# Kernel tuning notes

Hardware: AMD Instinct MI355X
Metric: run time of the kernel (lower is better)

The kernel has to match this reference:

```python
import jax, jax.numpy as jnp
import numpy as np

N, E, D, ED, L, B = 100000, 1600000, 128, 16, 5, 64
EPS = 1e-5


def _layer_norm(x, w, b):
    mu = jnp.mean(x, axis=-1, keepdims=True)
    var = jnp.mean((x - mu) ** 2, axis=-1, keepdims=True)
    return (x - mu) * jax.lax.rsqrt(var + EPS) * w + b


def setup_inputs() -> dict:
    key = jax.random.key(0)
    ks = jax.random.split(key, 10)
    sc = 0.05
    s = jax.random.normal(ks[0], (N, D), jnp.float32)
    edge_index = jax.random.randint(ks[1], (2, E), 0, N, dtype=jnp.int64)
    edge_attr = jax.random.normal(ks[2], (E, ED), jnp.float32)
    batch = jnp.sort(jax.random.randint(ks[3], (N,), 0, B, dtype=jnp.int64))
    return dict(
        s=s, edge_index=edge_index, edge_attr=edge_attr, batch=batch,
        ln_w=jnp.ones((L, D), jnp.float32),
        ln_b=jnp.zeros((L, D), jnp.float32),
        eW1=jax.random.normal(ks[4], (L, 2 * D + ED, ED), jnp.float32) * sc,
        eb1=jnp.zeros((L, ED), jnp.float32),
        eW2=jax.random.normal(ks[5], (L, ED, ED), jnp.float32) * sc,
        eb2=jnp.zeros((L, ED), jnp.float32),
        nW1=jax.random.normal(ks[6], (L, D + ED, D), jnp.float32) * sc,
        nb1=jnp.zeros((L, D), jnp.float32),
        nW2=jax.random.normal(ks[7], (L, D, D), jnp.float32) * sc,
        nb2=jnp.zeros((L, D), jnp.float32),
    )


def reference(s, edge_index, edge_attr, batch, ln_w, ln_b, eW1, eb1, eW2, eb2, nW1, nb1, nW2, nb2):
    src, dst = edge_index[0], edge_index[1]
    n = s.shape[0]
    num_layers = ln_w.shape[0]
    # scatter-mean denominator (in-degree, clamped to 1)
    deg = jax.ops.segment_sum(jnp.ones((edge_index.shape[1],), s.dtype), dst, num_segments=n)
    deg = jnp.maximum(deg, 1.0)[:, None]
    for i in range(num_layers):
        # per-node LayerNorm over feature dim (vector channel is None)
        s = _layer_norm(s, ln_w[i], ln_b[i])
        # edge message: gather endpoints, concat with edge_attr -> [E, 2D+ED]
        m = jnp.concatenate([s[src], s[dst], edge_attr], axis=-1)
        edge_attr = jax.nn.silu(m @ eW1[i] + eb1[i]) @ eW2[i] + eb2[i]
        # scatter-mean aggregate to destination nodes -> [N, ED]
        agg = jax.ops.segment_sum(edge_attr, dst, num_segments=n) / deg
        h = jnp.concatenate([s, agg], axis=-1)
        out = jax.nn.silu(h @ nW1[i] + nb1[i]) @ nW2[i] + nb2[i]  # discarded, as in original
    return s, edge_attr
```

## Files before the change

kernel.cpp:

```cpp
#include <hip/hip_runtime.h>

#define N_NODES 100000
#define N_EDGES 1600000
#define DIM     128
#define EDIM    16
#define NLAYERS 5

typedef unsigned short ushort_t;
typedef short bf16x8 __attribute__((ext_vector_type(8)));
typedef float f32x4  __attribute__((ext_vector_type(4)));

__device__ __forceinline__ ushort_t f2bf(float f) {
    union { float f; unsigned int i; } c; c.f = f;
    unsigned int r = c.i + 0x7fffu + ((c.i >> 16) & 1u);
    return (ushort_t)(r >> 16);
}
__device__ __forceinline__ float lo_bf(unsigned int w) {
    union { unsigned int i; float f; } c; c.i = w << 16; return c.f;
}
__device__ __forceinline__ float hi_bf(unsigned int w) {
    union { unsigned int i; float f; } c; c.i = w & 0xffff0000u; return c.f;
}
__device__ __forceinline__ unsigned int pk_bf16(float lo, float hi) {
    unsigned int r;
    asm("v_cvt_pk_bf16_f32 %0, %1, %2" : "=v"(r) : "v"(lo), "v"(hi));
    return r;
}
__device__ __forceinline__ bf16x8 pk8(f32x4 a, f32x4 b) {
    union { unsigned int w[4]; bf16x8 v; } c;
    c.w[0] = pk_bf16(a[0], a[1]); c.w[1] = pk_bf16(a[2], a[3]);
    c.w[2] = pk_bf16(b[0], b[1]); c.w[3] = pk_bf16(b[2], b[3]);
    return c.v;
}
__device__ __forceinline__ float fast_silu(float x) {
    return x * __builtin_amdgcn_rcpf(1.0f + __expf(-x));
}
__device__ __forceinline__ void lds_fence() {
    asm volatile("s_waitcnt lgkmcnt(0)" ::: "memory");
    __builtin_amdgcn_sched_barrier(0);
}

__global__ void swizzle_weights(const float* __restrict__ eW1,
                                const float* __restrict__ eW2,
                                ushort_t* __restrict__ w1s,
                                ushort_t* __restrict__ w2s) {
    int id = blockIdx.x * 256 + threadIdx.x;
    if (id >= NLAYERS * 10 * 64) return;
    int lane = id & 63;
    int t10 = id >> 6;
    int layer = t10 / 10, t = t10 % 10;
    int n = lane & 15, quad = lane >> 4;
    if (t < 9) {
        ushort_t* dst = w1s + ((size_t)(layer * 9 + t) * 64 + lane) * 8;
        #pragma unroll
        for (int j = 0; j < 8; ++j) {
            int k = t * 32 + quad * 8 + j;
            dst[j] = (k < 2 * DIM + EDIM)
                       ? f2bf(eW1[((size_t)layer * 272 + k) * 16 + n])
                       : (ushort_t)0;
        }
    } else {
        ushort_t* dst = w2s + ((size_t)layer * 64 + lane) * 8;
        #pragma unroll
        for (int j = 0; j < 8; ++j) {
            int k = quad * 8 + j;
            dst[j] = (k < EDIM) ? f2bf(eW2[((size_t)layer * 16 + k) * 16 + n])
                                : (ushort_t)0;
        }
    }
}

__global__ __launch_bounds__(256) void ln_uv(
        const float* __restrict__ sin, float* __restrict__ sout,
        const float* __restrict__ lnw, const float* __restrict__ lnb,
        const ushort_t* __restrict__ w1s,
        ushort_t* __restrict__ u_buf, ushort_t* __restrict__ v_buf,
        int l0, int l1, int lstr) {
    const int wv = threadIdx.x >> 6, lane = threadIdx.x & 63;
    const int m = lane & 15, quad = lane >> 4;
    const int tile = blockIdx.x * 4 + wv;
    if (tile >= N_NODES / 16) return;
    const int node = tile * 16 + m;

    float x[32];
    {
        const float* row = sin + (size_t)node * DIM + quad * 8;
        #pragma unroll
        for (int t = 0; t < 4; ++t) {
            f32x4 a = *(const f32x4*)(row + t * 32);
            f32x4 b = *(const f32x4*)(row + t * 32 + 4);
            #pragma unroll
            for (int j = 0; j < 4; ++j) { x[t * 8 + j] = a[j]; x[t * 8 + 4 + j] = b[j]; }
        }
    }

    for (int li = l0; li < l1; ++li) {
        float s = 0.f;
        #pragma unroll
        for (int k = 0; k < 32; ++k) s += x[k];
        s += __shfl_xor(s, 16); s += __shfl_xor(s, 32);
        float mu = s * (1.0f / DIM);
        float ss = 0.f;
        #pragma unroll
        for (int k = 0; k < 32; ++k) { float d = x[k] - mu; ss += d * d; }
        ss += __shfl_xor(ss, 16); ss += __shfl_xor(ss, 32);
        float rs = rsqrtf(ss * (1.0f / DIM) + 1e-5f);

        const float* w = lnw + (size_t)li * DIM + quad * 8;
        const float* b = lnb + (size_t)li * DIM + quad * 8;
        f32x4 au = {0.f, 0.f, 0.f, 0.f}, av = {0.f, 0.f, 0.f, 0.f};
        #pragma unroll
        for (int t = 0; t < 4; ++t) {
            f32x4 wa = *(const f32x4*)(w + t * 32), wb = *(const f32x4*)(w + t * 32 + 4);
            f32x4 ba = *(const f32x4*)(b + t * 32), bb = *(const f32x4*)(b + t * 32 + 4);
            #pragma unroll
            for (int j = 0; j < 4; ++j) {
                x[t * 8 + j]     = (x[t * 8 + j]     - mu) * rs * wa[j] + ba[j];
                x[t * 8 + 4 + j] = (x[t * 8 + 4 + j] - mu) * rs * wb[j] + bb[j];
            }
            f32x4 ya, yb;
            #pragma unroll
            for (int j = 0; j < 4; ++j) { ya[j] = x[t * 8 + j]; yb[j] = x[t * 8 + 4 + j]; }
            bf16x8 af = pk8(ya, yb);
            bf16x8 bu = *(const bf16x8*)(w1s + ((size_t)(li * 9 + t)     * 64 + lane) * 8);
            bf16x8 bv = *(const bf16x8*)(w1s + ((size_t)(li * 9 + 4 + t) * 64 + lane) * 8);
            au = __builtin_amdgcn_mfma_f32_16x16x32_bf16(bu, af, au, 0, 0, 0);
            av = __builtin_amdgcn_mfma_f32_16x16x32_bf16(bv, af, av, 0, 0, 0);
        }
        size_t rec = ((size_t)node * lstr + (li - l0)) * EDIM + quad * 4;
        uint2 tu; tu.x = pk_bf16(au[0], au[1]); tu.y = pk_bf16(au[2], au[3]);
        uint2 tv; tv.x = pk_bf16(av[0], av[1]); tv.y = pk_bf16(av[2], av[3]);
        *(uint2*)(u_buf + rec) = tu;
        *(uint2*)(v_buf + rec) = tv;
    }

    float* orow = sout + (size_t)node * DIM + quad * 8;
    #pragma unroll
    for (int t = 0; t < 4; ++t) {
        f32x4 a, b;
        #pragma unroll
        for (int j = 0; j < 4; ++j) { a[j] = x[t * 8 + j]; b[j] = x[t * 8 + 4 + j]; }
        *(f32x4*)(orow + t * 32) = a;
        *(f32x4*)(orow + t * 32 + 4) = b;
    }
}

template<int NL>
__global__ __launch_bounds__(256) void edge_fused(
        const float* __restrict__ ea_in, float* __restrict__ ea_out,
        const int* __restrict__ ei,
        const ushort_t* __restrict__ u_buf, const ushort_t* __restrict__ v_buf,
        const ushort_t* __restrict__ w1s, const ushort_t* __restrict__ w2s,
        const float* __restrict__ eb1, const float* __restrict__ eb2,
        int l0) {
    __shared__ ushort_t tbH[4][16 * 24];
    __shared__ ushort_t tbY[4][16 * 24];
    const int wv = threadIdx.x >> 6, lane = threadIdx.x & 63;
    const int m = lane & 15, quad = lane >> 4;

    bf16x8 w1f[NL], w2f[NL];
    f32x4 b1[NL], b2[NL];
    #pragma unroll
    for (int l = 0; l < NL; ++l) {
        w1f[l] = *(const bf16x8*)(w1s + (((size_t)(l0 + l) * 9 + 8) * 64 + lane) * 8);
        w2f[l] = *(const bf16x8*)(w2s + ((size_t)(l0 + l) * 64 + lane) * 8);
        #pragma unroll
        for (int r = 0; r < 4; ++r) {
            b1[l][r] = eb1[(l0 + l) * EDIM + quad * 4 + r];
            b2[l][r] = eb2[(l0 + l) * EDIM + quad * 4 + r];
        }
    }
    ushort_t* tlH = tbH[wv];
    ushort_t* tlY = tbY[wv];
    const bf16x8 zf = {0, 0, 0, 0, 0, 0, 0, 0};
    const f32x4 z4 = {0.f, 0.f, 0.f, 0.f};
    const int nTiles = N_EDGES / 64;
    const int stride = gridDim.x;

    int tile = blockIdx.x;
    if (tile >= nTiles) return;

    uint2 gu[NL], gv[NL];
    f32x4 ea_a = z4, ea_b = z4;
    int es_n, ed_n;
    {
        const int e0 = tile * 64 + wv * 16 + m;
        const int es = ei[e0];
        const int ed = ei[N_EDGES + e0];
        #pragma unroll
        for (int l = 0; l < NL; ++l) {
            gu[l] = *(const uint2*)(u_buf + ((size_t)es * NL + l) * EDIM + quad * 4);
            gv[l] = *(const uint2*)(v_buf + ((size_t)ed * NL + l) * EDIM + quad * 4);
        }
        if (quad < 2) {
            const float* ep = ea_in + (size_t)e0 * EDIM + quad * 8;
            ea_a = *(const f32x4*)ep; ea_b = *(const f32x4*)(ep + 4);
        }
        const int t1 = tile + stride;
        const int e1 = (t1 < nTiles ? t1 : tile) * 64 + wv * 16 + m;
        es_n = ei[e1];
        ed_n = ei[N_EDGES + e1];
    }

    for (; tile < nTiles; tile += stride) {
        const int tn = tile + stride;
        const bool hn = tn < nTiles;
        const int tc = hn ? tn : tile;

        uint2 gun[NL], gvn[NL];
        #pragma unroll
        for (int l = 0; l < NL; ++l) {
            gun[l] = *(const uint2*)(u_buf + ((size_t)es_n * NL + l) * EDIM + quad * 4);
            gvn[l] = *(const uint2*)(v_buf + ((size_t)ed_n * NL + l) * EDIM + quad * 4);
        }
        f32x4 ean_a = z4, ean_b = z4;
        {
            const int en = tc * 64 + wv * 16 + m;
            if (quad < 2) {
                const float* ep = ea_in + (size_t)en * EDIM + quad * 8;
                ean_a = *(const f32x4*)ep; ean_b = *(const f32x4*)(ep + 4);
            }
        }
        int es_nn, ed_nn;
        {
            const int t2 = tn + stride;
            const int e2 = (t2 < nTiles ? t2 : tc) * 64 + wv * 16 + m;
            es_nn = ei[e2];
            ed_nn = ei[N_EDGES + e2];
        }

        bf16x8 af = zf;
        if (quad < 2) af = pk8(ea_a, ea_b);

        f32x4 y = z4;
        #pragma unroll
        for (int l = 0; l < NL; ++l) {
            f32x4 acc = z4;
            acc = __builtin_amdgcn_mfma_f32_16x16x32_bf16(w1f[l], af, acc, 0, 0, 0);
            float x0 = acc[0] + lo_bf(gu[l].x) + lo_bf(gv[l].x) + b1[l][0];
            float x1 = acc[1] + hi_bf(gu[l].x) + hi_bf(gv[l].x) + b1[l][1];
            float x2 = acc[2] + lo_bf(gu[l].y) + lo_bf(gv[l].y) + b1[l][2];
            float x3 = acc[3] + hi_bf(gu[l].y) + hi_bf(gv[l].y) + b1[l][3];
            float h0 = fast_silu(x0);
            float h1 = fast_silu(x1);
            float h2 = fast_silu(x2);
            float h3 = fast_silu(x3);

            uint2 hw; hw.x = pk_bf16(h0, h1); hw.y = pk_bf16(h2, h3);
            *(uint2*)(tlH + m * 24 + quad * 4) = hw;
            lds_fence();
            bf16x8 hf = zf;
            if (quad < 2) hf = *(const bf16x8*)(tlH + m * 24 + quad * 8);

            f32x4 acc2 = z4;
            acc2 = __builtin_amdgcn_mfma_f32_16x16x32_bf16(w2f[l], hf, acc2, 0, 0, 0);
            y[0] = acc2[0] + b2[l][0];
            y[1] = acc2[1] + b2[l][1];
            y[2] = acc2[2] + b2[l][2];
            y[3] = acc2[3] + b2[l][3];

            if (l < NL - 1) {
                uint2 yw; yw.x = pk_bf16(y[0], y[1]); yw.y = pk_bf16(y[2], y[3]);
                *(uint2*)(tlY + m * 24 + quad * 4) = yw;
                lds_fence();
                af = zf;
                if (quad < 2) af = *(const bf16x8*)(tlY + m * 24 + quad * 8);
            }
        }
        const int e = tile * 64 + wv * 16 + m;
        *(f32x4*)(ea_out + (size_t)e * EDIM + quad * 4) = y;

        #pragma unroll
        for (int l = 0; l < NL; ++l) { gu[l] = gun[l]; gv[l] = gvn[l]; }
        ea_a = ean_a; ea_b = ean_b;
        es_n = es_nn; ed_n = ed_nn;
    }
}

extern "C" void kernel_launch(void* const* d_in, const int* in_sizes, int n_in,
                              void* d_out, int out_size, void* d_ws, size_t ws_size,
                              hipStream_t stream) {
    const float* s_in  = (const float*)d_in[0];
    const int*   ei    = (const int*)d_in[1];
    const float* ea_in = (const float*)d_in[2];
    const float* lnw = (const float*)d_in[4];
    const float* lnb = (const float*)d_in[5];
    const float* eW1 = (const float*)d_in[6];
    const float* eb1 = (const float*)d_in[7];
    const float* eW2 = (const float*)d_in[8];
    const float* eb2 = (const float*)d_in[9];

    float* out_s  = (float*)d_out;
    float* out_ea = (float*)d_out + (size_t)N_NODES * DIM;

    ushort_t* w1s = (ushort_t*)d_ws;
    ushort_t* w2s = w1s + (size_t)NLAYERS * 9 * 64 * 8;
    ushort_t* uv0 = w2s + (size_t)NLAYERS * 64 * 8;
    const size_t wWords  = (size_t)NLAYERS * 10 * 64 * 8;
    const size_t uvLayer = (size_t)N_NODES * EDIM;
    const size_t needFused = (wWords + 2 * (size_t)NLAYERS * uvLayer) * 2;
    const int lnGrid = (N_NODES / 16 + 3) / 4;
    const int eGrid = 4096;

    swizzle_weights<<<13, 256, 0, stream>>>(eW1, eW2, w1s, w2s);

    if (ws_size >= needFused) {
        ushort_t* u0 = uv0;
        ushort_t* v0 = u0 + (size_t)NLAYERS * uvLayer;
        ln_uv<<<lnGrid, 256, 0, stream>>>(s_in, out_s, lnw, lnb, w1s,
                                          u0, v0, 0, NLAYERS, NLAYERS);
        edge_fused<NLAYERS><<<eGrid, 256, 0, stream>>>(ea_in, out_ea, ei, u0, v0,
                                                       w1s, w2s, eb1, eb2, 0);
    } else {
        ushort_t* u0 = uv0;
        ushort_t* v0 = u0 + uvLayer;
        for (int l = 0; l < NLAYERS; ++l) {
            ln_uv<<<lnGrid, 256, 0, stream>>>(l == 0 ? s_in : out_s, out_s,
                                              lnw, lnb, w1s, u0, v0, l, l + 1, 1);
            edge_fused<1><<<eGrid, 256, 0, stream>>>(
                l == 0 ? ea_in : (const float*)out_ea, out_ea, ei, u0, v0,
                w1s, w2s, eb1, eb2, l);
        }
    }
}
```

Baseline: 434.9 us.

## Fold consecutive layer linear maps eW2·eW1_attr into combined weights

Precomputes the product of layer l's second edge linear (eW2) with layer l+1's edge-attr slice of eW1, plus the matching folded bias. The fused edge kernel then does one MFMA per layer transition instead of two, and drops one LDS round-trip and fence per layer. The folding is done once in the weight-swizzle kernel. The combined weight is rounded to bf16 after the fp32 product, which slightly changes numerics.

```diff
diff --git a/kernel.cpp b/kernel.cpp
--- a/kernel.cpp
+++ b/kernel.cpp
@@ -42,31 +42,59 @@
 
 __global__ void swizzle_weights(const float* __restrict__ eW1,
                                 const float* __restrict__ eW2,
+                                const float* __restrict__ eb1,
+                                const float* __restrict__ eb2,
                                 ushort_t* __restrict__ w1s,
-                                ushort_t* __restrict__ w2s) {
+                                ushort_t* __restrict__ w2s,
+                                ushort_t* __restrict__ wcs,
+                                float* __restrict__ bcs) {
     int id = blockIdx.x * 256 + threadIdx.x;
-    if (id >= NLAYERS * 10 * 64) return;
-    int lane = id & 63;
-    int t10 = id >> 6;
-    int layer = t10 / 10, t = t10 % 10;
-    int n = lane & 15, quad = lane >> 4;
-    if (t < 9) {
-        ushort_t* dst = w1s + ((size_t)(layer * 9 + t) * 64 + lane) * 8;
+    const int base = NLAYERS * 10 * 64;
+    if (id < base) {
+        int lane = id & 63;
+        int t10 = id >> 6;
+        int layer = t10 / 10, t = t10 % 10;
+        int n = lane & 15, quad = lane >> 4;
+        if (t < 9) {
+            ushort_t* dst = w1s + ((size_t)(layer * 9 + t) * 64 + lane) * 8;
+            #pragma unroll
+            for (int j = 0; j < 8; ++j) {
+                int k = t * 32 + quad * 8 + j;
+                dst[j] = (k < 2 * DIM + EDIM)
+                           ? f2bf(eW1[((size_t)layer * 272 + k) * 16 + n])
+                           : (ushort_t)0;
+            }
+        } else {
+            ushort_t* dst = w2s + ((size_t)layer * 64 + lane) * 8;
+            #pragma unroll
+            for (int j = 0; j < 8; ++j) {
+                int k = quad * 8 + j;
+                dst[j] = (k < EDIM) ? f2bf(eW2[((size_t)layer * 16 + k) * 16 + n])
+                                    : (ushort_t)0;
+            }
+        }
+    } else if (id < base + 4 * 64) {
+        int id2 = id - base;
+        int l = id2 >> 6;
+        int lane = id2 & 63, n = lane & 15, quad = lane >> 4;
+        ushort_t* dst = wcs + ((size_t)l * 64 + lane) * 8;
         #pragma unroll
         for (int j = 0; j < 8; ++j) {
-            int k = t * 32 + quad * 8 + j;
-            dst[j] = (k < 2 * DIM + EDIM)
-                       ? f2bf(eW1[((size_t)layer * 272 + k) * 16 + n])
-                       : (ushort_t)0;
-        }
-    } else {
-        ushort_t* dst = w2s + ((size_t)layer * 64 + lane) * 8;
-        #pragma unroll
-        for (int j = 0; j < 8; ++j) {
-            int k = quad * 8 + j;
-            dst[j] = (k < EDIM) ? f2bf(eW2[((size_t)layer * 16 + k) * 16 + n])
-                                : (ushort_t)0;
-        }
+            int r = quad * 8 + j;
+            float acc = 0.f;
+            if (r < EDIM)
+                for (int k = 0; k < EDIM; ++k)
+                    acc += eW2[((size_t)l * 16 + r) * 16 + k]
+                         * eW1[((size_t)(l + 1) * 272 + 256 + k) * 16 + n];
+            dst[j] = (r < EDIM) ? f2bf(acc) : (ushort_t)0;
+        }
+    } else if (id < base + 4 * 64 + 64) {
+        int id2 = id - base - 4 * 64;
+        int l = id2 >> 4, n = id2 & 15;
+        float acc = eb1[(l + 1) * 16 + n];
+        for (int k = 0; k < EDIM; ++k)
+            acc += eb2[l * 16 + k] * eW1[((size_t)(l + 1) * 272 + 256 + k) * 16 + n];
+        bcs[l * 16 + n] = acc;
     }
 }
 
@@ -151,27 +179,32 @@
         const int* __restrict__ ei,
         const ushort_t* __restrict__ u_buf, const ushort_t* __restrict__ v_buf,
         const ushort_t* __restrict__ w1s, const ushort_t* __restrict__ w2s,
+        const ushort_t* __restrict__ wcs, const float* __restrict__ bcs,
         const float* __restrict__ eb1, const float* __restrict__ eb2,
         int l0) {
     __shared__ ushort_t tbH[4][16 * 24];
-    __shared__ ushort_t tbY[4][16 * 24];
     const int wv = threadIdx.x >> 6, lane = threadIdx.x & 63;
     const int m = lane & 15, quad = lane >> 4;
 
-    bf16x8 w1f[NL], w2f[NL];
-    f32x4 b1[NL], b2[NL];
+    const bf16x8 w1f0 = *(const bf16x8*)(w1s + (((size_t)l0 * 9 + 8) * 64 + lane) * 8);
+    const bf16x8 w2f  = *(const bf16x8*)(w2s + ((size_t)(l0 + NL - 1) * 64 + lane) * 8);
+    bf16x8 wcf[NL > 1 ? NL - 1 : 1];
     #pragma unroll
-    for (int l = 0; l < NL; ++l) {
-        w1f[l] = *(const bf16x8*)(w1s + (((size_t)(l0 + l) * 9 + 8) * 64 + lane) * 8);
-        w2f[l] = *(const bf16x8*)(w2s + ((size_t)(l0 + l) * 64 + lane) * 8);
-        #pragma unroll
-        for (int r = 0; r < 4; ++r) {
-            b1[l][r] = eb1[(l0 + l) * EDIM + quad * 4 + r];
-            b2[l][r] = eb2[(l0 + l) * EDIM + quad * 4 + r];
-        }
-    }
+    for (int l = 1; l < NL; ++l)
+        wcf[l - 1] = *(const bf16x8*)(wcs + ((size_t)(l0 + l - 1) * 64 + lane) * 8);
+    f32x4 bx[NL], b2v;
+    #pragma unroll
+    for (int r = 0; r < 4; ++r) {
+        bx[0][r] = eb1[l0 * EDIM + quad * 4 + r];
+        b2v[r]   = eb2[(l0 + NL - 1) * EDIM + quad * 4 + r];
+    }
+    #pragma unroll
+    for (int l = 1; l < NL; ++l)
+        #pragma unroll
+        for (int r = 0; r < 4; ++r)
+            bx[l][r] = bcs[(l0 + l - 1) * EDIM + quad * 4 + r];
+
     ushort_t* tlH = tbH[wv];
-    ushort_t* tlY = tbY[wv];
     const bf16x8 zf = {0, 0, 0, 0, 0, 0, 0, 0};
     const f32x4 z4 = {0.f, 0.f, 0.f, 0.f};
     const int nTiles = N_EDGES / 64;
@@ -229,43 +262,42 @@
             ed_nn = ei[N_EDGES + e2];
         }
 
-        bf16x8 af = zf;
-        if (quad < 2) af = pk8(ea_a, ea_b);
-
-        f32x4 y = z4;
-        #pragma unroll
-        for (int l = 0; l < NL; ++l) {
-            f32x4 acc = z4;
-            acc = __builtin_amdgcn_mfma_f32_16x16x32_bf16(w1f[l], af, acc, 0, 0, 0);
-            float x0 = acc[0] + lo_bf(gu[l].x) + lo_bf(gv[l].x) + b1[l][0];
-            float x1 = acc[1] + hi_bf(gu[l].x) + hi_bf(gv[l].x) + b1[l][1];
-            float x2 = acc[2] + lo_bf(gu[l].y) + lo_bf(gv[l].y) + b1[l][2];
-            float x3 = acc[3] + hi_bf(gu[l].y) + hi_bf(gv[l].y) + b1[l][3];
-            float h0 = fast_silu(x0);
-            float h1 = fast_silu(x1);
-            float h2 = fast_silu(x2);
-            float h3 = fast_silu(x3);
-
-            uint2 hw; hw.x = pk_bf16(h0, h1); hw.y = pk_bf16(h2, h3);
+        f32x4 hv;
+        {
+            bf16x8 af = zf;
+            if (quad < 2) af = pk8(ea_a, ea_b);
+            f32x4 acc = __builtin_amdgcn_mfma_f32_16x16x32_bf16(w1f0, af, z4, 0, 0, 0);
+            hv[0] = fast_silu(acc[0] + lo_bf(gu[0].x) + lo_bf(gv[0].x) + bx[0][0]);
+            hv[1] = fast_silu(acc[1] + hi_bf(gu[0].x) + hi_bf(gv[0].x) + bx[0][1]);
+            hv[2] = fast_silu(acc[2] + lo_bf(gu[0].y) + lo_bf(gv[0].y) + bx[0][2]);
+            hv[3] = fast_silu(acc[3] + hi_bf(gu[0].y) + hi_bf(gv[0].y) + bx[0][3]);
+        }
+        #pragma unroll
+        for (int l = 1; l < NL; ++l) {
+            uint2 hw; hw.x = pk_bf16(hv[0], hv[1]); hw.y = pk_bf16(hv[2], hv[3]);
             *(uint2*)(tlH + m * 24 + quad * 4) = hw;
             lds_fence();
             bf16x8 hf = zf;
             if (quad < 2) hf = *(const bf16x8*)(tlH + m * 24 + quad * 8);
 
-            f32x4 acc2 = z4;
-            acc2 = __builtin_amdgcn_mfma_f32_16x16x32_bf16(w2f[l], hf, acc2, 0, 0, 0);
-            y[0] = acc2[0] + b2[l][0];
-            y[1] = acc2[1] + b2[l][1];
-            y[2] = acc2[2] + b2[l][2];
-            y[3] = acc2[3] + b2[l][3];
-
-            if (l < NL - 1) {
-                uint2 yw; yw.x = pk_bf16(y[0], y[1]); yw.y = pk_bf16(y[2], y[3]);
-                *(uint2*)(tlY + m * 24 + quad * 4) = yw;
-                lds_fence();
-                af = zf;
-                if (quad < 2) af = *(const bf16x8*)(tlY + m * 24 + quad * 8);
-            }
+            f32x4 acc = __builtin_amdgcn_mfma_f32_16x16x32_bf16(wcf[l - 1], hf, z4, 0, 0, 0);
+            hv[0] = fast_silu(acc[0] + lo_bf(gu[l].x) + lo_bf(gv[l].x) + bx[l][0]);
+            hv[1] = fast_silu(acc[1] + hi_bf(gu[l].x) + hi_bf(gv[l].x) + bx[l][1]);
+            hv[2] = fast_silu(acc[2] + lo_bf(gu[l].y) + lo_bf(gv[l].y) + bx[l][2]);
+            hv[3] = fast_silu(acc[3] + hi_bf(gu[l].y) + hi_bf(gv[l].y) + bx[l][3]);
+        }
+        f32x4 y;
+        {
+            uint2 hw; hw.x = pk_bf16(hv[0], hv[1]); hw.y = pk_bf16(hv[2], hv[3]);
+            *(uint2*)(tlH + m * 24 + quad * 4) = hw;
+            lds_fence();
+            bf16x8 hf = zf;
+            if (quad < 2) hf = *(const bf16x8*)(tlH + m * 24 + quad * 8);
+            f32x4 acc2 = __builtin_amdgcn_mfma_f32_16x16x32_bf16(w2f, hf, z4, 0, 0, 0);
+            y[0] = acc2[0] + b2v[0];
+            y[1] = acc2[1] + b2v[1];
+            y[2] = acc2[2] + b2v[2];
+            y[3] = acc2[3] + b2v[3];
         }
         const int e = tile * 64 + wv * 16 + m;
         *(f32x4*)(ea_out + (size_t)e * EDIM + quad * 4) = y;
@@ -295,14 +327,16 @@
 
     ushort_t* w1s = (ushort_t*)d_ws;
     ushort_t* w2s = w1s + (size_t)NLAYERS * 9 * 64 * 8;
-    ushort_t* uv0 = w2s + (size_t)NLAYERS * 64 * 8;
-    const size_t wWords  = (size_t)NLAYERS * 10 * 64 * 8;
+    ushort_t* wcs = w2s + (size_t)NLAYERS * 64 * 8;
+    float*    bcs = (float*)(wcs + 4 * 64 * 8);
+    ushort_t* uv0 = wcs + 4 * 64 * 8 + 128;
+    const size_t wWords  = (size_t)NLAYERS * 10 * 64 * 8 + 4 * 64 * 8 + 128;
     const size_t uvLayer = (size_t)N_NODES * EDIM;
     const size_t needFused = (wWords + 2 * (size_t)NLAYERS * uvLayer) * 2;
     const int lnGrid = (N_NODES / 16 + 3) / 4;
     const int eGrid = 4096;
 
-    swizzle_weights<<<13, 256, 0, stream>>>(eW1, eW2, w1s, w2s);
+    swizzle_weights<<<14, 256, 0, stream>>>(eW1, eW2, eb1, eb2, w1s, w2s, wcs, bcs);
 
     if (ws_size >= needFused) {
         ushort_t* u0 = uv0;
@@ -310,7 +344,8 @@
         ln_uv<<<lnGrid, 256, 0, stream>>>(s_in, out_s, lnw, lnb, w1s,
                                           u0, v0, 0, NLAYERS, NLAYERS);
         edge_fused<NLAYERS><<<eGrid, 256, 0, stream>>>(ea_in, out_ea, ei, u0, v0,
-                                                       w1s, w2s, eb1, eb2, 0);
+                                                       w1s, w2s, wcs, bcs,
+                                                       eb1, eb2, 0);
     } else {
         ushort_t* u0 = uv0;
         ushort_t* v0 = u0 + uvLayer;
@@ -319,7 +354,7 @@
                                               lnw, lnb, w1s, u0, v0, l, l + 1, 1);
             edge_fused<1><<<eGrid, 256, 0, stream>>>(
                 l == 0 ? ea_in : (const float*)out_ea, out_ea, ei, u0, v0,
-                w1s, w2s, eb1, eb2, l);
-        }
-    }
-}
+                w1s, w2s, wcs, bcs, eb1, eb2, l);
+        }
+    }
+}
```

After: 431.3 us. No clear change (-0.8%).
